# Kernel tuning notes

Hardware: AMD Instinct MI355X
Metric: run time of the kernel (lower is better)

Reference implementation:

```python
import jax, jax.numpy as jnp
import numpy as np
from jax import lax
from jax.scipy.special import logsumexp

N, M, B, T_MAX = 16, 64, 512, 4096


def setup_inputs() -> dict:
    key = jax.random.key(0)
    k1, k2, k3, k4, k5 = jax.random.split(key, 5)
    return {
        "x": jax.random.randint(k1, (B, T_MAX), 0, M),            # observation indices
        "T": jax.random.randint(k2, (B,), 1, T_MAX + 1),          # lengths in [1, T_max]
        "trans_logits": jax.random.normal(k3, (N, N), jnp.float32),
        "emiss_logits": jax.random.normal(k4, (N, M), jnp.float32),
        "prior_logits": jax.random.normal(k5, (N,), jnp.float32),
    }


def reference(x, T, trans_logits, emiss_logits, prior_logits):
    # Normalizations exactly as in the torch module
    log_A = jax.nn.log_softmax(trans_logits, axis=0)   # (N, N), columns normalized: A[i,k] = log p(i | k)
    log_E = jax.nn.log_softmax(emiss_logits, axis=1)   # (N, M)
    log_pi = jax.nn.log_softmax(prior_logits)          # (N,)

    # t = 0: log_alpha[b, i] = log_E[i, x[b,0]] + log_pi[i]
    alpha0 = log_E[:, x[:, 0]].T + log_pi              # (B, N)

    def step(alpha, x_t):
        # new[b, i] = log_E[i, x_t[b]] + logsumexp_k (log_A[i,k] + alpha[b,k])
        trans = logsumexp(log_A[None, :, :] + alpha[:, None, :], axis=2)  # (B, N)
        new = log_E[:, x_t].T + trans
        # carry full alpha; emit only per-step logsumexp to avoid (T,B,N) buffer
        return new, logsumexp(new, axis=1)

    ls0 = logsumexp(alpha0, axis=1)                    # (B,)
    _, ls_rest = lax.scan(step, alpha0, x[:, 1:].T)    # ls_rest: (T_max-1, B)
    log_sums = jnp.concatenate([ls0[None, :], ls_rest], axis=0)  # (T_max, B)

    # gather log p(x_{1..T_b}) at index T_b - 1 for each batch element
    log_probs = jnp.take_along_axis(log_sums.T, (T - 1)[:, None], axis=1)  # (B, 1)
    return jnp.exp(log_probs)


if __name__ == "__main__":
    out = reference(**setup_inputs())
    print(out.shape, out.dtype)
```

## Files before the change

### kernel.cpp

```cpp
#include <hip/hip_runtime.h>
#include <hip/hip_bf16.h>


#define NS    16
#define MOBS  64
#define SSH   5
#define NSEG  32

typedef float f32x4 __attribute__((ext_vector_type(4)));
typedef short s16x4 __attribute__((ext_vector_type(4)));

static __device__ __forceinline__ int imin(int a, int b){ return a < b ? a : b; }

static __device__ __forceinline__ unsigned short f2bf(float f){
  return __bfloat16_as_ushort(__float2bfloat16(f));
}
static __device__ __forceinline__ float b2f(unsigned short u){
  unsigned bits = ((unsigned)u) << 16;
  return __builtin_bit_cast(float, bits);
}

static __device__ __forceinline__ s16x4 pack_bf16x4(f32x4 C){
  unsigned r0, r1;
  asm("v_cvt_pk_bf16_f32 %0, %1, %2" : "=v"(r0) : "v"(C.x), "v"(C.y));
  asm("v_cvt_pk_bf16_f32 %0, %1, %2" : "=v"(r1) : "v"(C.z), "v"(C.w));
  uint2 pu; pu.x = r0; pu.y = r1;
  return __builtin_bit_cast(s16x4, pu);
}

#if __has_builtin(__builtin_amdgcn_mfma_f32_16x16x16bf16_1k)
static __device__ __forceinline__ f32x4 mfma16(s16x4 a, s16x4 b, f32x4 c){
  return __builtin_amdgcn_mfma_f32_16x16x16bf16_1k(a, b, c, 0, 0, 0);
}
#else
static __device__ __forceinline__ f32x4 mfma16(s16x4 a, s16x4 b, f32x4 c){
  f32x4 d;
  asm volatile("v_mfma_f32_16x16x16_bf16 %0, %1, %2, %3"
               : "=&v"(d) : "v"(a), "v"(b), "v"(c));
  return d;
}
#endif


__global__ void hmm_setup(const float* __restrict__ tl, const float* __restrict__ el,
                          const float* __restrict__ pl, float* __restrict__ ws,
                          unsigned short* __restrict__ g2)
{
  int m = blockIdx.x, t = threadIdx.x;
  __shared__ float Al[256];
  __shared__ float ev[16];
  if (t < 16){
    float mx = -3.0e38f;
    for (int i = 0; i < 16; ++i) mx = fmaxf(mx, tl[i*NS + t]);
    float sm = 0.f;
    for (int i = 0; i < 16; ++i) sm += expf(tl[i*NS + t] - mx);
    float inv = 1.f / sm;
    for (int i = 0; i < 16; ++i) Al[i*16 + t] = expf(tl[i*NS + t] - mx) * inv;
  } else if (t < 32){
    int i = t - 16;
    if (m < 64){
      float mx = -3.0e38f;
      for (int mm = 0; mm < MOBS; ++mm) mx = fmaxf(mx, el[i*MOBS + mm]);
      float sm = 0.f;
      for (int mm = 0; mm < MOBS; ++mm) sm += expf(el[i*MOBS + mm] - mx);
      float v = expf(el[i*MOBS + m] - mx) / sm;
      ev[i] = v;
      ws[m*16 + i] = v;
      g2[16640 + m*16 + i] = f2bf(v);
    } else ev[i] = 1.f;
  } else if (t < 48 && m == 64){
    int i = t - 32;
    float mx = -3.0e38f;
    for (int k = 0; k < 16; ++k) mx = fmaxf(mx, pl[k]);
    float sm = 0.f;
    for (int k = 0; k < 16; ++k) sm += expf(pl[k] - mx);
    ws[1024 + i] = expf(pl[i] - mx) / sm;
  }
  __syncthreads();
  int l = t >> 2, e = t & 3;
  int i = l & 15, col = ((l >> 4) << 2) + e;
  float acc;
  if (m == 64){
    acc = Al[i*16 + col];
  } else {
    acc = 0.f;
    #pragma unroll
    for (int k = 0; k < 16; ++k) acc += Al[i*16 + k] * ev[k] * Al[k*16 + col];
  }
  g2[(m*64 + l)*4 + e] = f2bf(acc);
}

template<bool MASK, bool REN>
static __device__ __forceinline__ void run_quad(
    int p0, int npair,
    const unsigned short* g2l, const unsigned short* etl,
    int lane4, int g4, int xp, s16x4& P, int& ce,
    s16x4 (&gf)[4], s16x4 (&ev)[4], s16x4 (&gfn)[4], s16x4 (&evn)[4])
{
  const f32x4 Z = {0.f, 0.f, 0.f, 0.f};
  #pragma unroll
  for (int p = 0; p < 4; ++p){
    int v = __builtin_amdgcn_readlane(xp, (p0 + 4 + p) & 63);
    gfn[p] = *(const s16x4*)&g2l[(v & 63)*256 + lane4];
    evn[p] = *(const s16x4*)&etl[((v >> 8) & 63)*16 + g4];

    f32x4 C = mfma16(gf[p], P, Z);
    C.x *= b2f((unsigned short)ev[p].x);
    C.y *= b2f((unsigned short)ev[p].y);
    C.z *= b2f((unsigned short)ev[p].z);
    C.w *= b2f((unsigned short)ev[p].w);

    bool commit = (!MASK) || (p0 + p < npair);
    if (REN && p == 3){
      float mm = fmaxf(fmaxf(C.x, C.y), fmaxf(C.z, C.w));
      mm = fmaxf(mm, __shfl_xor(mm, 16));
      mm = fmaxf(mm, __shfl_xor(mm, 32));
      int kk; (void)frexpf(mm, &kk);
      if (commit){
        C.x = ldexpf(C.x, -kk); C.y = ldexpf(C.y, -kk);
        C.z = ldexpf(C.z, -kk); C.w = ldexpf(C.w, -kk);
        ce += kk;
      }
    }
    if (commit){
      P = pack_bf16x4(C);
    }
  }
}

__global__ __launch_bounds__(512, 1) void hmm_seg(
    const int* __restrict__ x, const int* __restrict__ Tl,
    const unsigned short* __restrict__ g2,
    unsigned short* __restrict__ Q, int* __restrict__ CE,
    int TMAX, int XN)
{
  int tid  = threadIdx.x;
  int lane = tid & 63;
  int wid  = __builtin_amdgcn_readfirstlane(tid >> 6);
  int g = lane >> 4, j = lane & 15;
  int lane4 = lane * 4, g4 = g * 4;

  int gseg = blockIdx.x * 8 + wid;
  int b = gseg >> SSH, s = gseg & (NSEG - 1);

  int steps = __builtin_amdgcn_readfirstlane(Tl[b]) - 1;
  int L  = (steps + NSEG - 1) >> SSH;
  int lo = s * L;
  int n  = imin(steps - lo, L);

  unsigned short* Qout = Q + (size_t)gseg * 256;
  int* ceout = CE + gseg * NS;

  int s_lo = (blockIdx.x & 3) * 8;
  if (s_lo * L >= steps){
    if (g == 0) ceout[j] = 0;
    #pragma unroll
    for (int e = 0; e < 4; ++e){
      int k = 4*g + e;
      Qout[k*16 + j] = (k == j) ? (unsigned short)0x3F80 : (unsigned short)0;
    }
    return;
  }

  __shared__ unsigned short g2l[64*256];
  __shared__ unsigned short etl[1024];
  {
    const uint4* s1 = (const uint4*)g2;
    const uint4* s2 = (const uint4*)(g2 + 16640);
    uint4* d1 = (uint4*)g2l;
    uint4* d2 = (uint4*)etl;
    for (int i = tid; i < 2048; i += 512) d1[i] = s1[i];
    if (tid < 128) d2[tid] = s2[tid];
  }
  __syncthreads();

  if (n <= 0){
    if (g == 0) ceout[j] = 0;
    #pragma unroll
    for (int e = 0; e < 4; ++e){
      int k = 4*g + e;
      Qout[k*16 + j] = (k == j) ? (unsigned short)0x3F80 : (unsigned short)0;
    }
    return;
  }

  int npair = n >> 1, odd = n & 1;
  int xbase = b*TMAX + 1 + lo;

  int i0 = xbase + 2*lane;
  int xa = x[imin(i0,     XN - 1)] & 63;
  int xb = x[imin(i0 + 1, XN - 1)] & 63;
  int xp = xa | (xb << 8);

  s16x4 P;
  P.x = (4*g+0 == j) ? (short)0x3F80 : (short)0;
  P.y = (4*g+1 == j) ? (short)0x3F80 : (short)0;
  P.z = (4*g+2 == j) ? (short)0x3F80 : (short)0;
  P.w = (4*g+3 == j) ? (short)0x3F80 : (short)0;

  s16x4 gfA[4], gfB[4], evA[4], evB[4];
  #pragma unroll
  for (int p = 0; p < 4; ++p){
    int v = __builtin_amdgcn_readlane(xp, p);
    gfA[p] = *(const s16x4*)&g2l[(v & 63)*256 + lane4];
    evA[p] = *(const s16x4*)&etl[((v >> 8) & 63)*16 + g4];
  }

  int ce = 0, p0 = 0;
  while (p0 + 8 <= npair){
    run_quad<false,false>(p0,   npair, g2l, etl, lane4, g4, xp, P, ce, gfA, evA, gfB, evB);
    run_quad<false,true >(p0+4, npair, g2l, etl, lane4, g4, xp, P, ce, gfB, evB, gfA, evA);
    p0 += 8;
  }
  if (p0 < npair){
    run_quad<true,true>(p0, npair, g2l, etl, lane4, g4, xp, P, ce, gfA, evA, gfB, evB);
    if (p0 + 4 < npair)
      run_quad<true,true>(p0+4, npair, g2l, etl, lane4, g4, xp, P, ce, gfB, evB, gfA, evA);
  }

  if (odd){
    int v = __builtin_amdgcn_readlane(xp, (n - 1) >> 1);
    int xm = v & 63;
    s16x4 af  = *(const s16x4*)&g2[16384 + lane4];
    s16x4 evo = *(const s16x4*)&etl[xm*16 + g4];
    const f32x4 Z = {0.f,0.f,0.f,0.f};
    f32x4 C = mfma16(af, P, Z);
    C.x *= b2f((unsigned short)evo.x); C.y *= b2f((unsigned short)evo.y);
    C.z *= b2f((unsigned short)evo.z); C.w *= b2f((unsigned short)evo.w);
    P = pack_bf16x4(C);
  }

  if (g == 0) ceout[j] = ce;
  unsigned short pb[4] = {(unsigned short)P.x, (unsigned short)P.y,
                          (unsigned short)P.z, (unsigned short)P.w};
  #pragma unroll
  for (int e = 0; e < 4; ++e) Qout[(4*g + e)*16 + j] = pb[e];
}

__global__ __launch_bounds__(256) void hmm_comb(
    const int* __restrict__ x, const float* __restrict__ ws,
    const unsigned short* __restrict__ Q, const int* __restrict__ CE,
    float* __restrict__ out, int TMAX)
{
  int lane = threadIdx.x & 63;
  int w    = threadIdx.x >> 6;
  int b    = blockIdx.x * 4 + w;
  int k = lane & 15, r = lane >> 4;

  int x0 = x[b*TMAX];
  float u = ws[1024 + k] * ws[x0*16 + k];
  int ce_tot = 0;

  const unsigned short* qb = Q  + (size_t)b * NSEG * 256;
  const int*            cb = CE + b * NSEG * 16;

  s16x4 qq = *(const s16x4*)&qb[k*16 + 4*r];
  int4  cv = *(const int4*)&cb[4*r];

  for (int s = 0; s < NSEG; ++s){
    s16x4 qn; int4 cn;
    if (s + 1 < NSEG){
      qn = *(const s16x4*)&qb[(s+1)*256 + k*16 + 4*r];
      cn = *(const int4*)&cb[(s+1)*16 + 4*r];
    }
    int c0 = __builtin_amdgcn_readlane(cv.x, 0);
    float m0 = ldexpf(b2f((unsigned short)qq.x), cv.x - c0);
    float m1 = ldexpf(b2f((unsigned short)qq.y), cv.y - c0);
    float m2 = ldexpf(b2f((unsigned short)qq.z), cv.z - c0);
    float m3 = ldexpf(b2f((unsigned short)qq.w), cv.w - c0);

    float u0 = __shfl(u, 4*r + 0);
    float u1 = __shfl(u, 4*r + 1);
    float u2 = __shfl(u, 4*r + 2);
    float u3 = __shfl(u, 4*r + 3);
    float acc = m0*u0 + m1*u1 + m2*u2 + m3*u3;
    acc += __shfl_xor(acc, 16);
    acc += __shfl_xor(acc, 32);

    int ek; (void)frexpf(acc, &ek);
    int k0 = __builtin_amdgcn_readlane(ek, 0);
    u = ldexpf(acc, -k0);
    ce_tot += c0 + k0;

    qq = qn; cv = cn;
  }

  float sm = u;
  sm += __shfl_xor(sm, 1);
  sm += __shfl_xor(sm, 2);
  sm += __shfl_xor(sm, 4);
  sm += __shfl_xor(sm, 8);
  if (lane == 0) out[b] = ldexpf(sm, ce_tot);
}

extern "C" void kernel_launch(void* const* d_in, const int* in_sizes, int n_in,
                              void* d_out, int out_size, void* d_ws, size_t ws_size,
                              hipStream_t stream)
{
  (void)n_in; (void)out_size; (void)ws_size;
  const int*   x  = (const int*)  d_in[0];
  const int*   T  = (const int*)  d_in[1];
  const float* tl = (const float*)d_in[2];
  const float* el = (const float*)d_in[3];
  const float* pl = (const float*)d_in[4];
  int B    = in_sizes[1];
  int TMAX = in_sizes[0] / B;
  int XN   = B * TMAX;

  float* ws = (float*)d_ws;
  unsigned short* g2 = (unsigned short*)((char*)d_ws + 8192);
  unsigned short* Q  = (unsigned short*)((char*)d_ws + 49152);
  int* CE = (int*)((char*)d_ws + 49152 + (size_t)B * NSEG * 512);
  float* out = (float*)d_out;

  hipLaunchKernelGGL(hmm_setup, dim3(65),          dim3(256), 0, stream, tl, el, pl, ws, g2);
  hipLaunchKernelGGL(hmm_seg,   dim3(B*NSEG/8),    dim3(512), 0, stream, x, T, g2, Q, CE, TMAX, XN);
  hipLaunchKernelGGL(hmm_comb,  dim3(B/4),         dim3(256), 0, stream, x, ws, Q, CE, out, TMAX);
}
```

Before: 50.67 us.

## Read transition tables from global memory instead of LDS, shrink seg blocks

Drops the per-block staging of the 32KB pair-transition table and emission table into shared memory and reads them directly from global memory (L1/L2 cached), with emission factors now read as fp32 from the workspace. Blocks shrink from 8 to 4 waves with launch bounds allowing 8 blocks per CU, raising occupancy and removing the LDS fill and barrier. The early-exit for fully empty blocks is removed. The trade is higher latency per dependent load in the serial recurrence loop, and the change assumes ws already holds the fp32 emission table in the expected layout.

```diff
diff --git a/kernel.cpp b/kernel.cpp
--- a/kernel.cpp
+++ b/kernel.cpp
@@ -93,22 +93,20 @@
 template<bool MASK, bool REN>
 static __device__ __forceinline__ void run_quad(
     int p0, int npair,
-    const unsigned short* g2l, const unsigned short* etl,
+    const unsigned short* __restrict__ g2, const float* __restrict__ et,
     int lane4, int g4, int xp, s16x4& P, int& ce,
-    s16x4 (&gf)[4], s16x4 (&ev)[4], s16x4 (&gfn)[4], s16x4 (&evn)[4])
+    s16x4 (&gf)[4], f32x4 (&ev)[4], s16x4 (&gfn)[4], f32x4 (&evn)[4])
 {
   const f32x4 Z = {0.f, 0.f, 0.f, 0.f};
   #pragma unroll
   for (int p = 0; p < 4; ++p){
     int v = __builtin_amdgcn_readlane(xp, (p0 + 4 + p) & 63);
-    gfn[p] = *(const s16x4*)&g2l[(v & 63)*256 + lane4];
-    evn[p] = *(const s16x4*)&etl[((v >> 8) & 63)*16 + g4];
+    gfn[p] = *(const s16x4*)&g2[(v & 63)*256 + lane4];
+    evn[p] = *(const f32x4*)&et[((v >> 8) & 63)*16 + g4];
 
     f32x4 C = mfma16(gf[p], P, Z);
-    C.x *= b2f((unsigned short)ev[p].x);
-    C.y *= b2f((unsigned short)ev[p].y);
-    C.z *= b2f((unsigned short)ev[p].z);
-    C.w *= b2f((unsigned short)ev[p].w);
+    C.x *= ev[p].x; C.y *= ev[p].y;
+    C.z *= ev[p].z; C.w *= ev[p].w;
 
     bool commit = (!MASK) || (p0 + p < npair);
     if (REN && p == 3){
@@ -128,9 +126,9 @@
   }
 }
 
-__global__ __launch_bounds__(512, 1) void hmm_seg(
+__global__ __launch_bounds__(256, 8) void hmm_seg(
     const int* __restrict__ x, const int* __restrict__ Tl,
-    const unsigned short* __restrict__ g2,
+    const float* __restrict__ ws, const unsigned short* __restrict__ g2,
     unsigned short* __restrict__ Q, int* __restrict__ CE,
     int TMAX, int XN)
 {
@@ -140,7 +138,7 @@
   int g = lane >> 4, j = lane & 15;
   int lane4 = lane * 4, g4 = g * 4;
 
-  int gseg = blockIdx.x * 8 + wid;
+  int gseg = blockIdx.x * 4 + wid;
   int b = gseg >> SSH, s = gseg & (NSEG - 1);
 
   int steps = __builtin_amdgcn_readfirstlane(Tl[b]) - 1;
@@ -150,29 +148,6 @@
 
   unsigned short* Qout = Q + (size_t)gseg * 256;
   int* ceout = CE + gseg * NS;
-
-  int s_lo = (blockIdx.x & 3) * 8;
-  if (s_lo * L >= steps){
-    if (g == 0) ceout[j] = 0;
-    #pragma unroll
-    for (int e = 0; e < 4; ++e){
-      int k = 4*g + e;
-      Qout[k*16 + j] = (k == j) ? (unsigned short)0x3F80 : (unsigned short)0;
-    }
-    return;
-  }
-
-  __shared__ unsigned short g2l[64*256];
-  __shared__ unsigned short etl[1024];
-  {
-    const uint4* s1 = (const uint4*)g2;
-    const uint4* s2 = (const uint4*)(g2 + 16640);
-    uint4* d1 = (uint4*)g2l;
-    uint4* d2 = (uint4*)etl;
-    for (int i = tid; i < 2048; i += 512) d1[i] = s1[i];
-    if (tid < 128) d2[tid] = s2[tid];
-  }
-  __syncthreads();
 
   if (n <= 0){
     if (g == 0) ceout[j] = 0;
@@ -192,41 +167,43 @@
   int xb = x[imin(i0 + 1, XN - 1)] & 63;
   int xp = xa | (xb << 8);
 
+  const float* et = ws;
+
   s16x4 P;
   P.x = (4*g+0 == j) ? (short)0x3F80 : (short)0;
   P.y = (4*g+1 == j) ? (short)0x3F80 : (short)0;
   P.z = (4*g+2 == j) ? (short)0x3F80 : (short)0;
   P.w = (4*g+3 == j) ? (short)0x3F80 : (short)0;
 
-  s16x4 gfA[4], gfB[4], evA[4], evB[4];
+  s16x4 gfA[4], gfB[4];
+  f32x4 evA[4], evB[4];
   #pragma unroll
   for (int p = 0; p < 4; ++p){
     int v = __builtin_amdgcn_readlane(xp, p);
-    gfA[p] = *(const s16x4*)&g2l[(v & 63)*256 + lane4];
-    evA[p] = *(const s16x4*)&etl[((v >> 8) & 63)*16 + g4];
+    gfA[p] = *(const s16x4*)&g2[(v & 63)*256 + lane4];
+    evA[p] = *(const f32x4*)&et[((v >> 8) & 63)*16 + g4];
   }
 
   int ce = 0, p0 = 0;
   while (p0 + 8 <= npair){
-    run_quad<false,false>(p0,   npair, g2l, etl, lane4, g4, xp, P, ce, gfA, evA, gfB, evB);
-    run_quad<false,true >(p0+4, npair, g2l, etl, lane4, g4, xp, P, ce, gfB, evB, gfA, evA);
+    run_quad<false,false>(p0,   npair, g2, et, lane4, g4, xp, P, ce, gfA, evA, gfB, evB);
+    run_quad<false,true >(p0+4, npair, g2, et, lane4, g4, xp, P, ce, gfB, evB, gfA, evA);
     p0 += 8;
   }
   if (p0 < npair){
-    run_quad<true,true>(p0, npair, g2l, etl, lane4, g4, xp, P, ce, gfA, evA, gfB, evB);
+    run_quad<true,true>(p0, npair, g2, et, lane4, g4, xp, P, ce, gfA, evA, gfB, evB);
     if (p0 + 4 < npair)
-      run_quad<true,true>(p0+4, npair, g2l, etl, lane4, g4, xp, P, ce, gfB, evB, gfA, evA);
+      run_quad<true,true>(p0+4, npair, g2, et, lane4, g4, xp, P, ce, gfB, evB, gfA, evA);
   }
 
   if (odd){
     int v = __builtin_amdgcn_readlane(xp, (n - 1) >> 1);
     int xm = v & 63;
-    s16x4 af  = *(const s16x4*)&g2[16384 + lane4];
-    s16x4 evo = *(const s16x4*)&etl[xm*16 + g4];
+    s16x4 af = *(const s16x4*)&g2[16384 + lane4];
+    f32x4 evo = *(const f32x4*)&et[xm*16 + g4];
     const f32x4 Z = {0.f,0.f,0.f,0.f};
     f32x4 C = mfma16(af, P, Z);
-    C.x *= b2f((unsigned short)evo.x); C.y *= b2f((unsigned short)evo.y);
-    C.z *= b2f((unsigned short)evo.z); C.w *= b2f((unsigned short)evo.w);
+    C.x *= evo.x; C.y *= evo.y; C.z *= evo.z; C.w *= evo.w;
     P = pack_bf16x4(C);
   }
 
@@ -314,6 +291,6 @@
   float* out = (float*)d_out;
 
   hipLaunchKernelGGL(hmm_setup, dim3(65),          dim3(256), 0, stream, tl, el, pl, ws, g2);
-  hipLaunchKernelGGL(hmm_seg,   dim3(B*NSEG/8),    dim3(512), 0, stream, x, T, g2, Q, CE, TMAX, XN);
+  hipLaunchKernelGGL(hmm_seg,   dim3(B*NSEG/4),    dim3(256), 0, stream, x, T, ws, g2, Q, CE, TMAX, XN);
   hipLaunchKernelGGL(hmm_comb,  dim3(B/4),         dim3(256), 0, stream, x, ws, Q, CE, out, TMAX);
 }
```

Result: slower. 70.29 us (+38.7%).
